# Performance work log

Hardware: AMD Instinct MI355X
Metric: run time of the kernel (lower is better)

## Reference

```python
import jax, jax.numpy as jnp
import numpy as np

N_E = 8192
DIM = 256
BETA = 0.25


def _l2norm(x, eps=1e-12):
    # matches F.normalize(p=2, dim=-1): x / max(||x||, eps)
    n = jnp.sqrt(jnp.sum(x * x, axis=-1, keepdims=True))
    return x / jnp.maximum(n, eps)


def setup_inputs() -> dict:
    key = jax.random.key(0)
    k1, k2 = jax.random.split(key)
    z = jax.random.normal(k1, (8, 1024, DIM), dtype=jnp.float32)
    embedding_weight = jax.random.normal(k2, (N_E, DIM), dtype=jnp.float32)
    return {"z": z, "embedding_weight": embedding_weight}


def reference(z, embedding_weight):
    z = _l2norm(z)                                   # [B,S,D]
    zf = z.reshape(-1, DIM)                          # [N,D]
    embed_norm = _l2norm(embedding_weight)           # [n_e,D]
    # d = ||z||^2 + ||e||^2 - 2 z.e  -> [N, n_e]
    d = (jnp.sum(zf * zf, axis=1, keepdims=True)
         + jnp.sum(embed_norm * embed_norm, axis=1)
         - 2.0 * jnp.einsum('bd,nd->bn', zf, embed_norm))
    encoding_indices = jnp.argmin(d, axis=1).reshape(z.shape[:-1])  # [B,S]
    z_q = embedding_weight[encoding_indices]          # gather raw codes
    z_q = _l2norm(z_q)                                # [B,S,D]
    loss = (BETA * jnp.mean((jax.lax.stop_gradient(z_q) - z) ** 2)
            + jnp.mean((z_q - jax.lax.stop_gradient(z)) ** 2))
    z_q = z + jax.lax.stop_gradient(z_q - z)          # straight-through
    return z_q, loss, encoding_indices
```

## Files before the change

kernel.cpp:

```cpp
#include <hip/hip_runtime.h>
#include <cfloat>
#include <math.h>

#define DIM    256
#define N_TOK  8192
#define N_E    8192
#define NSEG   512
#define MARGIN 0.016f

typedef __attribute__((ext_vector_type(8))) short bf16x8;
typedef __attribute__((ext_vector_type(4))) float f32x4;

__device__ __forceinline__ unsigned short f2bf(float f) {
    unsigned u = __float_as_uint(f);
    unsigned r = u + 0x7fff + ((u >> 16) & 1);
    return (unsigned short)(r >> 16);
}
__device__ __forceinline__ unsigned fkey(float f) {
    unsigned u = __float_as_uint(f);
    return (u & 0x80000000u) ? ~u : (u | 0x80000000u);
}

__global__ __launch_bounds__(256) void l2norm_rows(const float* __restrict__ in,
                                                   float* __restrict__ out,
                                                   unsigned short* __restrict__ outb,
                                                   float* __restrict__ nsq) {
    const int lane = threadIdx.x & 63;
    const int row  = (blockIdx.x << 2) + (threadIdx.x >> 6);
    const float4 v = *(const float4*)(in + row * DIM + lane * 4);
    float s = v.x * v.x + v.y * v.y + v.z * v.z + v.w * v.w;
#pragma unroll
    for (int off = 1; off < 64; off <<= 1) s += __shfl_xor(s, off, 64);
    const float inv = 1.0f / fmaxf(sqrtf(s), 1e-12f);
    const float4 o = make_float4(v.x * inv, v.y * inv, v.z * inv, v.w * inv);
    *(float4*)(out + row * DIM + lane * 4) = o;
    ushort4 ob; ob.x = f2bf(o.x); ob.y = f2bf(o.y); ob.z = f2bf(o.z); ob.w = f2bf(o.w);
    *(ushort4*)(outb + row * DIM + lane * 4) = ob;
    if (nsq) {
        float e2 = o.x * o.x + o.y * o.y + o.z * o.z + o.w * o.w;
#pragma unroll
        for (int off = 1; off < 64; off <<= 1) e2 += __shfl_xor(e2, off, 64);
        if (lane == 0) nsq[row] = e2;
    }
}

__global__ __launch_bounds__(256, 2) void mfma_dist(const unsigned short* __restrict__ zb,
                                                    const unsigned short* __restrict__ eb,
                                                    const float* __restrict__ e2,
                                                    float* __restrict__ segM) {
    __shared__ __align__(16) unsigned short As[128][32];
    __shared__ __align__(16) unsigned short Bs[128][32];
    __shared__ __align__(16) float sm[8][128];

    const int tid  = threadIdx.x;
    const int lane = tid & 63;
    const int wave = tid >> 6;
    const int wm = wave & 1, wn = wave >> 1;
    const int row0 = (blockIdx.x & 63) * 128;
    const int col0 = (blockIdx.x >> 6) * 128;

    f32x4 acc[4][4];
#pragma unroll
    for (int ci = 0; ci < 4; ci++)
#pragma unroll
        for (int zi = 0; zi < 4; zi++) acc[ci][zi] = (f32x4){0.f, 0.f, 0.f, 0.f};

    const int srow  = lane >> 2;
    const int skoff = (lane & 3) * 8;
    const unsigned short* gA = zb + (row0 + wave * 32 + srow) * DIM + skoff;
    const unsigned short* gB = eb + (col0 + wave * 32 + srow) * DIM + skoff;

    for (int kc = 0; kc < DIM / 32; kc++) {
        __syncthreads();
#pragma unroll
        for (int j = 0; j < 2; j++) {
            __builtin_amdgcn_global_load_lds(
                (const __attribute__((address_space(1))) unsigned int*)(gA + j * 16 * DIM + kc * 32),
                (__attribute__((address_space(3))) unsigned int*)&As[wave * 32 + j * 16][0],
                16, 0, 0);
            __builtin_amdgcn_global_load_lds(
                (const __attribute__((address_space(1))) unsigned int*)(gB + j * 16 * DIM + kc * 32),
                (__attribute__((address_space(3))) unsigned int*)&Bs[wave * 32 + j * 16][0],
                16, 0, 0);
        }
        __syncthreads();
        const int fr = lane & 15, q = lane >> 4;
        bf16x8 cf[4], zfr[4];
#pragma unroll
        for (int i = 0; i < 4; i++) cf[i]  = *(const bf16x8*)&Bs[wn * 64 + i * 16 + fr][q * 8];
#pragma unroll
        for (int i = 0; i < 4; i++) zfr[i] = *(const bf16x8*)&As[wm * 64 + i * 16 + fr][q * 8];
#pragma unroll
        for (int ci = 0; ci < 4; ci++)
#pragma unroll
            for (int zi = 0; zi < 4; zi++)
                acc[ci][zi] = __builtin_amdgcn_mfma_f32_16x16x32_bf16(cf[ci], zfr[zi], acc[ci][zi], 0, 0, 0);
    }

    const int fr = lane & 15, q = lane >> 4;
    float4 e2q[4];
#pragma unroll
    for (int ci = 0; ci < 4; ci++)
        e2q[ci] = *(const float4*)&e2[col0 + wn * 64 + ci * 16 + q * 4];
#pragma unroll
    for (int ci = 0; ci < 4; ci++) {
#pragma unroll
        for (int zi = 0; zi < 4; zi++) {
            const float t0 = fmaf(-2.0f, acc[ci][zi][0], e2q[ci].x);
            const float t1 = fmaf(-2.0f, acc[ci][zi][1], e2q[ci].y);
            const float t2 = fmaf(-2.0f, acc[ci][zi][2], e2q[ci].z);
            const float t3 = fmaf(-2.0f, acc[ci][zi][3], e2q[ci].w);
            float mm = fminf(fminf(t0, t1), fminf(t2, t3));
            mm = fminf(mm, __shfl_xor(mm, 16, 64));
            mm = fminf(mm, __shfl_xor(mm, 32, 64));
            if (q == 0) sm[wn * 4 + ci][wm * 64 + zi * 16 + fr] = mm;
        }
    }
    __syncthreads();
    {
        const int rl = tid & 127, part = tid >> 7;
        float4 v;
        v.x = sm[part * 4 + 0][rl]; v.y = sm[part * 4 + 1][rl];
        v.z = sm[part * 4 + 2][rl]; v.w = sm[part * 4 + 3][rl];
        *(float4*)&segM[(size_t)(row0 + rl) * NSEG + (col0 >> 4) + part * 4] = v;
    }
}

__global__ __launch_bounds__(256) void select_rescore(const float* __restrict__ segM,
                                                      const float* __restrict__ en,
                                                      const float* __restrict__ e2,
                                                      float* zq,
                                                      float* out_base,
                                                      float* __restrict__ pl) {
    const int lane = threadIdx.x & 63;
    const int row  = (blockIdx.x << 2) + (threadIdx.x >> 6);
    const float4* p = (const float4*)(segM + (size_t)row * NSEG);
    const float4 v0 = p[lane];
    const float4 v1 = p[64 + lane];
    const float vv[8] = {v0.x, v0.y, v0.z, v0.w, v1.x, v1.y, v1.z, v1.w};
    float m = vv[0];
#pragma unroll
    for (int j = 1; j < 8; j++) m = fminf(m, vv[j]);
#pragma unroll
    for (int off = 1; off < 64; off <<= 1) m = fminf(m, __shfl_xor(m, off, 64));
    const float thr = m + MARGIN;

    const int q = lane >> 4, f = lane & 15;
    const float4* zp = (const float4*)(zq + (size_t)row * DIM);
    float4 z4[4];
#pragma unroll
    for (int j = 0; j < 4; j++) z4[j] = zp[j * 16 + f];

    unsigned long long pk = ~0ull;
#pragma unroll
    for (int j = 0; j < 8; j++) {
        unsigned long long bal = __ballot(vv[j] <= thr);
        while (bal) {
            const int l = __ffsll(bal) - 1;
            bal &= bal - 1;
            const int seg = (j < 4) ? (l * 4 + j) : (256 + l * 4 + (j - 4));
#pragma unroll
            for (int g = 0; g < 4; g++) {
                const int col = seg * 16 + g * 4 + q;
                const float4* ep = (const float4*)(en + (size_t)col * DIM);
                float s = 0.f;
#pragma unroll
                for (int jj = 0; jj < 4; jj++) {
                    const float4 ev = ep[jj * 16 + f];
                    s = fmaf(z4[jj].x, ev.x, s); s = fmaf(z4[jj].y, ev.y, s);
                    s = fmaf(z4[jj].z, ev.z, s); s = fmaf(z4[jj].w, ev.w, s);
                }
#pragma unroll
                for (int off = 1; off < 16; off <<= 1) s += __shfl_xor(s, off, 64);
                const float d = fmaf(-2.0f, s, e2[col]);
                const unsigned long long key =
                    ((unsigned long long)fkey(d) << 32) | (unsigned)col;
                if (key < pk) pk = key;
            }
        }
    }
#pragma unroll
    for (int off = 16; off < 64; off <<= 1) {
        const unsigned long long o = __shfl_xor(pk, off, 64);
        if (o < pk) pk = o;
    }
    const int i = (int)(pk & 0xffffffffu);

    const float4 qv = *(const float4*)(en + (size_t)i * DIM + lane * 4);
    const float4 zv = *(const float4*)(zq + (size_t)row * DIM + lane * 4);
    const float dx = qv.x - zv.x, dy = qv.y - zv.y, dz = qv.z - zv.z, dw = qv.w - zv.w;
    float s = dx * dx + dy * dy + dz * dz + dw * dw;
    *(float4*)(zq + (size_t)row * DIM + lane * 4) = qv;
#pragma unroll
    for (int off = 1; off < 64; off <<= 1) s += __shfl_xor(s, off, 64);
    if (lane == 0) {
        pl[row] = s;
        out_base[N_TOK * DIM + 1 + row] = (float)i;
    }
}

__global__ __launch_bounds__(1024) void finalize_loss(const float* __restrict__ pl,
                                                      float* __restrict__ out) {
    __shared__ float sw[16];
    const int t = threadIdx.x;
    float s = 0.f;
#pragma unroll
    for (int j = 0; j < 8; j++) s += pl[t + j * 1024];
#pragma unroll
    for (int off = 1; off < 64; off <<= 1) s += __shfl_xor(s, off, 64);
    if ((t & 63) == 0) sw[t >> 6] = s;
    __syncthreads();
    if (t < 16) {
        float v = sw[t];
#pragma unroll
        for (int off = 1; off < 16; off <<= 1) v += __shfl_xor(v, off, 64);
        if (t == 0) out[N_TOK * DIM] = v * (1.25f / 2097152.0f);
    }
}

extern "C" void kernel_launch(void* const* d_in, const int* in_sizes, int n_in,
                              void* d_out, int out_size, void* d_ws, size_t ws_size,
                              hipStream_t stream) {
    const float* z   = (const float*)d_in[0];
    const float* emb = (const float*)d_in[1];
    float* out = (float*)d_out;
    char* ws = (char*)d_ws;

    float*          en   = (float*)(ws);
    unsigned short* eb   = (unsigned short*)(ws + 8388608);
    unsigned short* zb   = (unsigned short*)(ws + 12582912);
    float*          e2   = (float*)(ws + 16777216);
    float*          segM = (float*)(ws + 16809984);
    float*          pl   = (float*)(ws + 33587200);

    l2norm_rows<<<N_E / 4, 256, 0, stream>>>(emb, en, eb, e2);
    l2norm_rows<<<N_TOK / 4, 256, 0, stream>>>(z, out, zb, nullptr);
    mfma_dist<<<64 * 64, 256, 0, stream>>>(zb, eb, e2, segM);
    select_rescore<<<N_TOK / 4, 256, 0, stream>>>(segM, en, e2, out, out, pl);
    finalize_loss<<<1, 1024, 0, stream>>>(pl, out);
}
```

Baseline: 152.7 us.

## Double-buffer LDS in distance GEMM, fuse l2norm launches, tighten rescore margin

The MFMA distance kernel now uses two LDS buffers, so the async global-to-LDS loads for the next K chunk are issued before the MFMAs on the current chunk, with one barrier per chunk instead of two. The two row-normalisation launches are merged into a single grid covering both the codebook and the tokens. The rescore margin is halved, so fewer candidate segments are rescored in fp32. A smaller margin raises the risk that bf16 rounding error picks the wrong argmin, and the double buffer doubles LDS use per block.

```diff
diff --git a/kernel.cpp b/kernel.cpp
--- a/kernel.cpp
+++ b/kernel.cpp
@@ -6,7 +6,7 @@
 #define N_TOK  8192
 #define N_E    8192
 #define NSEG   512
-#define MARGIN 0.016f
+#define MARGIN 0.008f
 
 typedef __attribute__((ext_vector_type(8))) short bf16x8;
 typedef __attribute__((ext_vector_type(4))) float f32x4;
@@ -21,12 +21,19 @@
     return (u & 0x80000000u) ? ~u : (u | 0x80000000u);
 }
 
-__global__ __launch_bounds__(256) void l2norm_rows(const float* __restrict__ in,
-                                                   float* __restrict__ out,
-                                                   unsigned short* __restrict__ outb,
-                                                   float* __restrict__ nsq) {
+__global__ __launch_bounds__(256) void l2norm_all(const float* __restrict__ z,
+                                                  const float* __restrict__ emb,
+                                                  float* __restrict__ zn,
+                                                  unsigned short* __restrict__ zb,
+                                                  float* __restrict__ en,
+                                                  unsigned short* __restrict__ eb,
+                                                  float* __restrict__ e2) {
     const int lane = threadIdx.x & 63;
-    const int row  = (blockIdx.x << 2) + (threadIdx.x >> 6);
+    const bool isE = blockIdx.x < (N_E / 4);
+    const int row = (isE ? blockIdx.x : blockIdx.x - N_E / 4) * 4 + (threadIdx.x >> 6);
+    const float* in = isE ? emb : z;
+    float* out = isE ? en : zn;
+    unsigned short* outb = isE ? eb : zb;
     const float4 v = *(const float4*)(in + row * DIM + lane * 4);
     float s = v.x * v.x + v.y * v.y + v.z * v.z + v.w * v.w;
 #pragma unroll
@@ -36,11 +43,11 @@
     *(float4*)(out + row * DIM + lane * 4) = o;
     ushort4 ob; ob.x = f2bf(o.x); ob.y = f2bf(o.y); ob.z = f2bf(o.z); ob.w = f2bf(o.w);
     *(ushort4*)(outb + row * DIM + lane * 4) = ob;
-    if (nsq) {
-        float e2 = o.x * o.x + o.y * o.y + o.z * o.z + o.w * o.w;
-#pragma unroll
-        for (int off = 1; off < 64; off <<= 1) e2 += __shfl_xor(e2, off, 64);
-        if (lane == 0) nsq[row] = e2;
+    if (isE) {
+        float q = o.x * o.x + o.y * o.y + o.z * o.z + o.w * o.w;
+#pragma unroll
+        for (int off = 1; off < 64; off <<= 1) q += __shfl_xor(q, off, 64);
+        if (lane == 0) e2[row] = q;
     }
 }
 
@@ -48,8 +55,8 @@
                                                     const unsigned short* __restrict__ eb,
                                                     const float* __restrict__ e2,
                                                     float* __restrict__ segM) {
-    __shared__ __align__(16) unsigned short As[128][32];
-    __shared__ __align__(16) unsigned short Bs[128][32];
+    __shared__ __align__(16) unsigned short As[2][128][32];
+    __shared__ __align__(16) unsigned short Bs[2][128][32];
     __shared__ __align__(16) float sm[8][128];
 
     const int tid  = threadIdx.x;
@@ -58,6 +65,7 @@
     const int wm = wave & 1, wn = wave >> 1;
     const int row0 = (blockIdx.x & 63) * 128;
     const int col0 = (blockIdx.x >> 6) * 128;
+    const int fr = lane & 15, q = lane >> 4;
 
     f32x4 acc[4][4];
 #pragma unroll
@@ -70,34 +78,43 @@
     const unsigned short* gA = zb + (row0 + wave * 32 + srow) * DIM + skoff;
     const unsigned short* gB = eb + (col0 + wave * 32 + srow) * DIM + skoff;
 
-    for (int kc = 0; kc < DIM / 32; kc++) {
-        __syncthreads();
+    auto stage = [&](int buf, int kcn) {
 #pragma unroll
         for (int j = 0; j < 2; j++) {
             __builtin_amdgcn_global_load_lds(
-                (const __attribute__((address_space(1))) unsigned int*)(gA + j * 16 * DIM + kc * 32),
-                (__attribute__((address_space(3))) unsigned int*)&As[wave * 32 + j * 16][0],
+                (const __attribute__((address_space(1))) unsigned int*)(gA + j * 16 * DIM + kcn * 32),
+                (__attribute__((address_space(3))) unsigned int*)&As[buf][wave * 32 + j * 16][0],
                 16, 0, 0);
             __builtin_amdgcn_global_load_lds(
-                (const __attribute__((address_space(1))) unsigned int*)(gB + j * 16 * DIM + kc * 32),
-                (__attribute__((address_space(3))) unsigned int*)&Bs[wave * 32 + j * 16][0],
+                (const __attribute__((address_space(1))) unsigned int*)(gB + j * 16 * DIM + kcn * 32),
+                (__attribute__((address_space(3))) unsigned int*)&Bs[buf][wave * 32 + j * 16][0],
                 16, 0, 0);
         }
-        __syncthreads();
-        const int fr = lane & 15, q = lane >> 4;
+    };
+    auto compute = [&](int buf) {
         bf16x8 cf[4], zfr[4];
 #pragma unroll
-        for (int i = 0; i < 4; i++) cf[i]  = *(const bf16x8*)&Bs[wn * 64 + i * 16 + fr][q * 8];
-#pragma unroll
-        for (int i = 0; i < 4; i++) zfr[i] = *(const bf16x8*)&As[wm * 64 + i * 16 + fr][q * 8];
+        for (int i = 0; i < 4; i++) cf[i]  = *(const bf16x8*)&Bs[buf][wn * 64 + i * 16 + fr][q * 8];
+#pragma unroll
+        for (int i = 0; i < 4; i++) zfr[i] = *(const bf16x8*)&As[buf][wm * 64 + i * 16 + fr][q * 8];
 #pragma unroll
         for (int ci = 0; ci < 4; ci++)
 #pragma unroll
             for (int zi = 0; zi < 4; zi++)
                 acc[ci][zi] = __builtin_amdgcn_mfma_f32_16x16x32_bf16(cf[ci], zfr[zi], acc[ci][zi], 0, 0, 0);
-    }
-
-    const int fr = lane & 15, q = lane >> 4;
+    };
+
+    stage(0, 0);
+#pragma unroll
+    for (int kc = 0; kc < 8; kc += 2) {
+        __syncthreads();
+        stage(1, kc + 1);
+        compute(0);
+        __syncthreads();
+        if (kc + 2 < 8) stage(0, kc + 2);
+        compute(1);
+    }
+
     float4 e2q[4];
 #pragma unroll
     for (int ci = 0; ci < 4; ci++)
@@ -233,8 +250,7 @@
     float*          segM = (float*)(ws + 16809984);
     float*          pl   = (float*)(ws + 33587200);
 
-    l2norm_rows<<<N_E / 4, 256, 0, stream>>>(emb, en, eb, e2);
-    l2norm_rows<<<N_TOK / 4, 256, 0, stream>>>(z, out, zb, nullptr);
+    l2norm_all<<<(N_E + N_TOK) / 4, 256, 0, stream>>>(z, emb, out, zb, en, eb, e2);
     mfma_dist<<<64 * 64, 256, 0, stream>>>(zb, eb, e2, segM);
     select_rescore<<<N_TOK / 4, 256, 0, stream>>>(segM, en, e2, out, out, pl);
     finalize_loss<<<1, 1024, 0, stream>>>(pl, out);
```

New measurement: 148.2 us. -2.9%, faster.
